# Kernel optimization log

Hardware: AMD Instinct MI355X
Metric: run time of the kernel (lower is better)

Reference implementation:

```python
import jax, jax.numpy as jnp
import numpy as np

V, B, P = 32, 128, 256   # views/directions, batch, max points per diagram
J = 75                   # n_elements (structure elements)
NF = 32                  # n_filters (= directions)
S2 = 25                  # stage_2_out
NU = 0.1
BN_EPS = 1e-5


def _transform(births, lifetimes):
    """UpperDiagonalThresholdedLogTransform(nu=0.1) on (birth, death) points."""
    deaths = births + lifetimes + 0.01
    inv = jnp.asarray(1.0 / np.sqrt(2.0), births.dtype)
    x = (births + deaths) * inv          # rotated 1st coord
    y = (deaths - births) * inv          # rotated 2nd coord (persistence), > 0
    y = jnp.where(y <= NU, jnp.log(y / NU) * NU + NU, y)
    return jnp.stack([x, y], axis=-1)    # [V,B,P,2]


def _batchnorm(x, gamma, beta, axis):
    mean = x.mean(axis=axis, keepdims=True)
    var = x.var(axis=axis, keepdims=True)  # biased, training-mode BN
    return (x - mean) / jnp.sqrt(var + BN_EPS) * gamma + beta


def setup_inputs() -> dict:
    key = jax.random.key(0)
    ks = jax.random.split(key, 20)
    inp = {
        "births": jax.random.uniform(ks[0], (V, B, P), jnp.float32),
        "lifetimes": jax.random.uniform(ks[1], (V, B, P), jnp.float32),
        "mask": jax.random.randint(ks[2], (V, B, P), 0, 2).astype(jnp.int32),
        # SLayerPHT params (one SLayer per view)
        "centers": jax.random.uniform(ks[3], (V, J, 2), jnp.float32),
        "sharpness": 4.0 + 0.1 * jax.random.normal(ks[4], (V, J, 2), jnp.float32),
        # stage_1: Conv1d(3->NF, k=1, no bias), Conv1d(NF->8, k=1, no bias)
        "w1": 0.1 * jax.random.normal(ks[5], (V, NF, 3), jnp.float32),
        "w2": 0.1 * jax.random.normal(ks[6], (V, 8, NF), jnp.float32),
        # stage_2: Linear(J->S2), BN(S2), Linear(S2->S2)
        "l1_w": 0.1 * jax.random.normal(ks[7], (V, S2, J), jnp.float32),
        "l1_b": 0.1 * jax.random.normal(ks[8], (V, S2), jnp.float32),
        "bn1_g": jnp.ones((V, S2), jnp.float32),
        "bn1_b": jnp.zeros((V, S2), jnp.float32),
        "l2_w": 0.1 * jax.random.normal(ks[9], (V, S2, S2), jnp.float32),
        "l2_b": 0.1 * jax.random.normal(ks[10], (V, S2), jnp.float32),
        # linear_1: Linear(V*S2 -> 500) + BN(500); linear_2: Linear(500 -> 200)
        "fc1_w": 0.05 * jax.random.normal(ks[11], (500, V * S2), jnp.float32),
        "fc1_b": 0.05 * jax.random.normal(ks[12], (500,), jnp.float32),
        "bn2_g": jnp.ones((500,), jnp.float32),
        "bn2_b": jnp.zeros((500,), jnp.float32),
        "fc2_w": 0.05 * jax.random.normal(ks[13], (200, 500), jnp.float32),
        "fc2_b": 0.05 * jax.random.normal(ks[14], (200,), jnp.float32),
    }
    return inp


def reference(births, lifetimes, mask, centers, sharpness, w1, w2,
              l1_w, l1_b, bn1_g, bn1_b, l2_w, l2_b,
              fc1_w, fc1_b, bn2_g, bn2_b, fc2_w, fc2_b):
    q = _transform(births, lifetimes)                 # [V,B,P,2]
    m = mask.astype(q.dtype)                          # [V,B,P]
    # SLayer: z[v,b,j] = sum_p m * exp(-sum_d s[v,j,d]^2 (q[v,b,p,d]-c[v,j,d])^2)
    s2 = sharpness * sharpness                        # [V,J,2]
    qa = jnp.concatenate([q * q, q, jnp.ones_like(q[..., :1])], axis=-1)  # [V,B,P,5]
    ca = jnp.concatenate([s2, -2.0 * s2 * centers,
                          (s2 * centers * centers).sum(-1, keepdims=True)], axis=-1)  # [V,J,5]
    d2 = jnp.einsum('vbpk,vjk->vbpj', qa, ca)         # squared weighted distance
    z = jnp.einsum('vbpj,vbp->vbj', jnp.exp(-d2), m)  # [V,B,J]
    # neighbor-direction stacking (n_neighbor_directions=1, cyclic): [i-1, i, i+1]
    zn = jnp.stack([jnp.roll(z, 1, axis=0), z, jnp.roll(z, -1, axis=0)], axis=2)  # [V,B,3,J]
    # stage_1: two 1x1 conv1d (no bias), then max over channels
    h = jnp.einsum('vbcj,vfc->vbfj', zn, w1)          # [V,B,NF,J]
    h = jnp.einsum('vbfj,vgf->vbgj', h, w2)           # [V,B,8,J]
    h = h.max(axis=2)                                 # [V,B,J]
    # stage_2: Linear -> BN(train) -> Linear -> ReLU (Dropout = eval identity)
    u = jnp.einsum('vbj,voj->vbo', h, l1_w) + l1_b[:, None, :]   # [V,B,S2]
    u = _batchnorm(u, bn1_g[:, None, :], bn1_b[:, None, :], axis=1)
    u = jnp.einsum('vbo,vpo->vbp', u, l2_w) + l2_b[:, None, :]
    u = jax.nn.relu(u)
    x = u.transpose(1, 0, 2).reshape(B, V * S2)       # torch.cat(x, 1)
    x = x @ fc1_w.T + fc1_b
    x = _batchnorm(x, bn2_g, bn2_b, axis=0)
    x = x @ fc2_w.T + fc2_b                           # [B,200]
    return x
```

## Files before the change

### kernel.cpp

```cpp
#include <hip/hip_runtime.h>

#define V 32
#define B 128
#define P 256
#define J 75
#define NF 32
#define S2 25
#define N1 500

__global__ __launch_bounds__(256) void slayer_kernel(
    const float* __restrict__ births,
    const float* __restrict__ lifetimes,
    const int* __restrict__ mask,
    const float* __restrict__ centers,
    const float* __restrict__ sharpness,
    float* __restrict__ z,
    float* __restrict__ acc_out)
{
    const int vb = blockIdx.x;
    const int v  = vb >> 7;
    const int tid = threadIdx.x;
    const int lane = tid & 63;

    {
        const int base = vb * 16;
        if (tid < 16 && base + tid < N1 * B) acc_out[base + tid] = 0.f;
    }

    __shared__ float4 pts[P];
    __shared__ int cnt;
    __shared__ float part[8 * J];

    if (tid == 0) cnt = 0;
    __syncthreads();

    const float inv = 0.70710678118654752f;
    {
        const int gi = vb * P + tid;
        float b0 = births[gi];
        float l0 = lifetimes[gi];
        int   m  = mask[gi];
        float d  = b0 + l0 + 0.01f;
        float x  = (b0 + d) * inv;
        float y  = (d - b0) * inv;
        if (y <= 0.1f) y = __logf(y * 10.0f) * 0.1f + 0.1f;

        bool keep = (m != 0);
        unsigned long long bal = __ballot(keep);
        unsigned long long lt  = (1ull << lane) - 1ull;
        int prefix = __popcll(bal & lt);
        int total  = __popcll(bal);
        int base = 0;
        if (lane == 0) base = atomicAdd(&cnt, total);
        base = __shfl(base, 0, 64);
        if (keep) pts[base + prefix] = make_float4(x, y, x * x, y * y);
    }
    __syncthreads();

    const int n = cnt;
    const int pid = tid >> 5;
    const int t32 = tid & 31;
    if (t32 < 25) {
        const int j0 = t32 * 3;
        float k0[3], k1[3], k2[3], k3[3], kc[3];
        #pragma unroll
        for (int c = 0; c < 3; ++c) {
            const int cj = (v * J + j0 + c) * 2;
            float cx = centers[cj + 0];
            float cy = centers[cj + 1];
            float sx = sharpness[cj + 0];
            float sy = sharpness[cj + 1];
            float s2x = sx * sx, s2y = sy * sy;
            k0[c] = -s2x;
            k1[c] = -s2y;
            k2[c] = 2.0f * s2x * cx;
            k3[c] = 2.0f * s2y * cy;
            kc[c] = -(s2x * cx * cx + s2y * cy * cy);
        }
        float a0 = 0.f, a1 = 0.f, a2 = 0.f;
        const int p0 = (n * pid) >> 3;
        const int p1 = (n * (pid + 1)) >> 3;
        #pragma unroll 2
        for (int p = p0; p < p1; ++p) {
            float4 a = pts[p];
            float d0 = fmaf(k0[0], a.z, kc[0]);
            d0 = fmaf(k1[0], a.w, d0); d0 = fmaf(k2[0], a.x, d0); d0 = fmaf(k3[0], a.y, d0);
            float d1 = fmaf(k0[1], a.z, kc[1]);
            d1 = fmaf(k1[1], a.w, d1); d1 = fmaf(k2[1], a.x, d1); d1 = fmaf(k3[1], a.y, d1);
            float d2 = fmaf(k0[2], a.z, kc[2]);
            d2 = fmaf(k1[2], a.w, d2); d2 = fmaf(k2[2], a.x, d2); d2 = fmaf(k3[2], a.y, d2);
            a0 += __expf(d0);
            a1 += __expf(d1);
            a2 += __expf(d2);
        }
        part[pid * J + j0 + 0] = a0;
        part[pid * J + j0 + 1] = a1;
        part[pid * J + j0 + 2] = a2;
    }
    __syncthreads();

    if (tid < J) {
        float s = 0.f;
        #pragma unroll
        for (int q = 0; q < 8; ++q) s += part[q * J + tid];
        z[vb * J + tid] = s;
    }
}

__global__ __launch_bounds__(1024) void stage2_kernel(
    const float* __restrict__ z,
    const float* __restrict__ w1,
    const float* __restrict__ w2,
    const float* __restrict__ l1_w,
    const float* __restrict__ l1_b,
    const float* __restrict__ bn1_g,
    const float* __restrict__ bn1_b,
    const float* __restrict__ l2_w,
    const float* __restrict__ l2_b,
    const float* __restrict__ fc1_w,
    float* __restrict__ acc_out)
{
    const int v   = blockIdx.x;
    const int tid = threadIdx.x;
    const int vm  = (v + V - 1) & (V - 1);
    const int vp  = (v + 1) & (V - 1);

    __shared__ float wcomb[8][3];
    __shared__ float l1ws[S2 * J];
    __shared__ float l1bs[S2];
    __shared__ float wl2[S2 * S2];
    __shared__ float l2bs[S2];
    __shared__ float hs[B * J];
    __shared__ float us[B * S2];
    __shared__ float xs[S2 * B];
    __shared__ float fw[N1 * S2];
    __shared__ float sred[32 * S2], ssred[32 * S2];
    __shared__ float sc[S2], sh[S2];

    if (tid < 24) {
        int g = tid / 3, c = tid - g * 3;
        const float* w2r = w2 + v * 8 * NF + g * NF;
        const float* w1c = w1 + v * NF * 3 + c;
        float s = 0.f;
        #pragma unroll
        for (int f = 0; f < NF; ++f) s += w2r[f] * w1c[f * 3];
        wcomb[g][c] = s;
    }
    for (int i = tid; i < S2 * J;  i += 1024) l1ws[i] = l1_w[v * S2 * J + i];
    for (int i = tid; i < S2 * S2; i += 1024) wl2[i]  = l2_w[v * S2 * S2 + i];
    for (int i = tid; i < N1 * S2; i += 1024) {
        int nn = i / S2, p = i - nn * S2;
        fw[i] = fc1_w[nn * (V * S2) + v * S2 + p];
    }
    if (tid < S2) { l1bs[tid] = l1_b[v * S2 + tid]; l2bs[tid] = l2_b[v * S2 + tid]; }
    __syncthreads();

    for (int t = tid; t < B * J; t += 1024) {
        float a0 = z[vm * (B * J) + t];
        float a1 = z[v  * (B * J) + t];
        float a2 = z[vp * (B * J) + t];
        float hm = -3.4e38f;
        #pragma unroll
        for (int g = 0; g < 8; ++g) {
            float s = wcomb[g][0] * a0 + wcomb[g][1] * a1 + wcomb[g][2] * a2;
            hm = fmaxf(hm, s);
        }
        hs[t] = hm;
    }
    __syncthreads();

    for (int t = tid; t < S2 * B; t += 1024) {
        int o = t >> 7;
        int b = t & 127;
        float acc = l1bs[o];
        const float* hrow = hs + b * J;
        const float* wrow = l1ws + o * J;
        #pragma unroll 5
        for (int j = 0; j < J; ++j) acc += hrow[j] * wrow[j];
        us[b * S2 + o] = acc;
    }
    __syncthreads();

    if (tid < 32 * S2) {
        int c = tid / S2;
        int o = tid - c * S2;
        float s = 0.f, ss = 0.f;
        #pragma unroll
        for (int b = c * 4; b < c * 4 + 4; ++b) {
            float x = us[b * S2 + o];
            s += x; ss += x * x;
        }
        sred[tid] = s; ssred[tid] = ss;
    }
    __syncthreads();

    if (tid < S2) {
        float s = 0.f, ss = 0.f;
        #pragma unroll
        for (int c = 0; c < 32; ++c) { s += sred[c * S2 + tid]; ss += ssred[c * S2 + tid]; }
        float mean = s * (1.f / B);
        float var  = ss * (1.f / B) - mean * mean;
        float istd = rsqrtf(var + 1e-5f);
        float g  = bn1_g[v * S2 + tid];
        float be = bn1_b[v * S2 + tid];
        sc[tid] = g * istd;
        sh[tid] = be - mean * g * istd;
    }
    __syncthreads();

    for (int i = tid; i < B * S2; i += 1024) {
        int o = i % S2;
        us[i] = us[i] * sc[o] + sh[o];
    }
    __syncthreads();

    for (int t = tid; t < S2 * B; t += 1024) {
        int p = t >> 7;
        int b = t & 127;
        float acc = l2bs[p];
        const float* urow = us + b * S2;
        const float* wrow = wl2 + p * S2;
        #pragma unroll
        for (int o = 0; o < S2; ++o) acc += urow[o] * wrow[o];
        xs[p * B + b] = fmaxf(acc, 0.f);
    }
    __syncthreads();

    for (int t = tid; t < N1 * B; t += 1024) {
        int nn = t >> 7;
        int b  = t & 127;
        const float* fr = fw + nn * S2;
        const float* xc = xs + b;
        float s = 0.f;
        #pragma unroll
        for (int p = 0; p < S2; ++p) s += fr[p] * xc[p * B];
        atomicAdd(&acc_out[nn * B + b], s);
    }
}

__global__ __launch_bounds__(256) void bn2_fc2_kernel(
    const float* __restrict__ acc_in,
    const float* __restrict__ fc1_b,
    const float* __restrict__ bn2_g,
    const float* __restrict__ bn2_b,
    const float* __restrict__ fc2_w,
    const float* __restrict__ fc2_b,
    float* __restrict__ out)
{
    const int k0  = blockIdx.x * 2;
    const int tid = threadIdx.x;

    __shared__ float w0s[N1], w1s[N1];
    __shared__ float fbs[N1];
    __shared__ float sred[2 * N1], ssred[2 * N1];
    __shared__ float scl[N1], shs[N1];
    __shared__ float pr0[B], pr1[B];

    for (int i = tid; i < N1; i += 256) {
        w0s[i] = fc2_w[k0 * N1 + i];
        w1s[i] = fc2_w[(k0 + 1) * N1 + i];
        fbs[i] = fc1_b[i];
    }
    __syncthreads();

    for (int idx = tid; idx < 2 * N1; idx += 256) {
        int nn = idx >> 1;
        int c  = idx & 1;
        const float* ap = acc_in + nn * B + c * 64;
        float fb = fbs[nn];
        float s = 0.f, ss = 0.f;
        #pragma unroll 8
        for (int j = 0; j < 64; ++j) {
            float x = ap[j] + fb;
            s += x; ss += x * x;
        }
        sred[idx] = s; ssred[idx] = ss;
    }
    __syncthreads();

    for (int nn = tid; nn < N1; nn += 256) {
        float s  = sred[2 * nn] + sred[2 * nn + 1];
        float ss = ssred[2 * nn] + ssred[2 * nn + 1];
        float mean = s * (1.f / B);
        float var  = ss * (1.f / B) - mean * mean;
        float istd = rsqrtf(var + 1e-5f);
        float g  = bn2_g[nn];
        float be = bn2_b[nn];
        scl[nn] = g * istd;
        shs[nn] = be - mean * g * istd;
    }
    __syncthreads();

    const int kk = tid >> 7;
    const int b  = tid & 127;
    float a0 = 0.f, a1 = 0.f;
    for (int nn = kk * 250; nn < kk * 250 + 250; ++nn) {
        float y = (acc_in[nn * B + b] + fbs[nn]) * scl[nn] + shs[nn];
        a0 += y * w0s[nn];
        a1 += y * w1s[nn];
    }
    if (kk == 1) { pr0[b] = a0; pr1[b] = a1; }
    __syncthreads();

    if (kk == 0) {
        out[b * 200 + k0]     = a0 + pr0[b] + fc2_b[k0];
        out[b * 200 + k0 + 1] = a1 + pr1[b] + fc2_b[k0 + 1];
    }
}

extern "C" void kernel_launch(void* const* d_in, const int* in_sizes, int n_in,
                              void* d_out, int out_size, void* d_ws, size_t ws_size,
                              hipStream_t stream) {
    const float* births    = (const float*)d_in[0];
    const float* lifetimes = (const float*)d_in[1];
    const int*   mask      = (const int*)d_in[2];
    const float* centers   = (const float*)d_in[3];
    const float* sharpness = (const float*)d_in[4];
    const float* w1        = (const float*)d_in[5];
    const float* w2        = (const float*)d_in[6];
    const float* l1_w      = (const float*)d_in[7];
    const float* l1_b      = (const float*)d_in[8];
    const float* bn1_g     = (const float*)d_in[9];
    const float* bn1_b     = (const float*)d_in[10];
    const float* l2_w      = (const float*)d_in[11];
    const float* l2_b      = (const float*)d_in[12];
    const float* fc1_w     = (const float*)d_in[13];
    const float* fc1_b     = (const float*)d_in[14];
    const float* bn2_g     = (const float*)d_in[15];
    const float* bn2_b     = (const float*)d_in[16];
    const float* fc2_w     = (const float*)d_in[17];
    const float* fc2_b     = (const float*)d_in[18];
    float* out = (float*)d_out;

    float* ws  = (float*)d_ws;
    float* z   = ws;
    float* acc = ws + 307200;

    slayer_kernel <<<V * B, 256, 0, stream>>>(births, lifetimes, mask, centers,
                                              sharpness, z, acc);
    stage2_kernel <<<V, 1024, 0, stream>>>(z, w1, w2, l1_w, l1_b, bn1_g, bn1_b,
                                           l2_w, l2_b, fc1_w, acc);
    bn2_fc2_kernel<<<100, 256, 0, stream>>>(acc, fc1_b, bn2_g, bn2_b,
                                            fc2_w, fc2_b, out);
}
```

Baseline: 173.0 us.

## Move fc1 out of per-view stage2 into separate fc1+BN and fc2 kernels

Stage2 now writes the per-view ReLU outputs to a transposed global buffer instead of doing its fc1 slice with 64K atomicAdds per block over 32 blocks. A new 250-block kernel computes fc1 for two output neurons each, including the full-batch BN via wave shuffles. A separate 200-block kernel does fc2. This removes atomics, the accumulator zeroing and the large per-view fc1 weight staging, and spreads the fc1 work over many more blocks, at the cost of an extra launch and an extra global round trip.

```diff
diff --git a/kernel.cpp b/kernel.cpp
--- a/kernel.cpp
+++ b/kernel.cpp
@@ -14,18 +14,12 @@
     const int* __restrict__ mask,
     const float* __restrict__ centers,
     const float* __restrict__ sharpness,
-    float* __restrict__ z,
-    float* __restrict__ acc_out)
+    float* __restrict__ z)
 {
     const int vb = blockIdx.x;
     const int v  = vb >> 7;
     const int tid = threadIdx.x;
     const int lane = tid & 63;
-
-    {
-        const int base = vb * 16;
-        if (tid < 16 && base + tid < N1 * B) acc_out[base + tid] = 0.f;
-    }
 
     __shared__ float4 pts[P];
     __shared__ int cnt;
@@ -117,8 +111,7 @@
     const float* __restrict__ bn1_b,
     const float* __restrict__ l2_w,
     const float* __restrict__ l2_b,
-    const float* __restrict__ fc1_w,
-    float* __restrict__ acc_out)
+    float* __restrict__ xT)
 {
     const int v   = blockIdx.x;
     const int tid = threadIdx.x;
@@ -132,8 +125,6 @@
     __shared__ float l2bs[S2];
     __shared__ float hs[B * J];
     __shared__ float us[B * S2];
-    __shared__ float xs[S2 * B];
-    __shared__ float fw[N1 * S2];
     __shared__ float sred[32 * S2], ssred[32 * S2];
     __shared__ float sc[S2], sh[S2];
 
@@ -148,10 +139,6 @@
     }
     for (int i = tid; i < S2 * J;  i += 1024) l1ws[i] = l1_w[v * S2 * J + i];
     for (int i = tid; i < S2 * S2; i += 1024) wl2[i]  = l2_w[v * S2 * S2 + i];
-    for (int i = tid; i < N1 * S2; i += 1024) {
-        int nn = i / S2, p = i - nn * S2;
-        fw[i] = fc1_w[nn * (V * S2) + v * S2 + p];
-    }
     if (tid < S2) { l1bs[tid] = l1_b[v * S2 + tid]; l2bs[tid] = l2_b[v * S2 + tid]; }
     __syncthreads();
 
@@ -222,90 +209,116 @@
         const float* wrow = wl2 + p * S2;
         #pragma unroll
         for (int o = 0; o < S2; ++o) acc += urow[o] * wrow[o];
-        xs[p * B + b] = fmaxf(acc, 0.f);
-    }
-    __syncthreads();
-
-    for (int t = tid; t < N1 * B; t += 1024) {
-        int nn = t >> 7;
-        int b  = t & 127;
-        const float* fr = fw + nn * S2;
-        const float* xc = xs + b;
-        float s = 0.f;
-        #pragma unroll
-        for (int p = 0; p < S2; ++p) s += fr[p] * xc[p * B];
-        atomicAdd(&acc_out[nn * B + b], s);
-    }
-}
-
-__global__ __launch_bounds__(256) void bn2_fc2_kernel(
-    const float* __restrict__ acc_in,
+        acc = fmaxf(acc, 0.f);
+        xT[(v * S2 + p) * B + b] = acc;
+    }
+}
+
+__global__ __launch_bounds__(256) void fc1_bn2_kernel(
+    const float* __restrict__ xT,
+    const float* __restrict__ fc1_w,
     const float* __restrict__ fc1_b,
     const float* __restrict__ bn2_g,
     const float* __restrict__ bn2_b,
+    float* __restrict__ y1n)
+{
+    const int n0  = blockIdx.x * 2;
+    const int tid = threadIdx.x;
+    const int kk  = tid >> 7;
+    const int b   = tid & 127;
+    const int K   = V * S2;
+
+    __shared__ float wsm[2][V * S2];
+    __shared__ float pr0[B], pr1[B];
+    __shared__ float red[2][2][2];
+
+    for (int i = tid; i < 2 * K; i += 256) {
+        int ni = i / K;
+        int k  = i - ni * K;
+        wsm[ni][k] = fc1_w[(n0 + ni) * K + k];
+    }
+    __syncthreads();
+
+    float a0 = 0.f, a1 = 0.f;
+    {
+        const float* xp = xT + kk * 400 * B + b;
+        const float* w0 = wsm[0] + kk * 400;
+        const float* w1p = wsm[1] + kk * 400;
+        for (int k = 0; k < 400; ++k) {
+            float xv = xp[k * B];
+            a0 += xv * w0[k];
+            a1 += xv * w1p[k];
+        }
+    }
+
+    if (kk == 1) { pr0[b] = a0; pr1[b] = a1; }
+    __syncthreads();
+
+    float t0 = 0.f, t1 = 0.f;
+    if (kk == 0) {
+        t0 = a0 + pr0[b] + fc1_b[n0];
+        t1 = a1 + pr1[b] + fc1_b[n0 + 1];
+        const int wave = tid >> 6;
+        const int lane = tid & 63;
+        float s0 = t0, q0 = t0 * t0;
+        float s1 = t1, q1 = t1 * t1;
+        #pragma unroll
+        for (int off = 32; off > 0; off >>= 1) {
+            s0 += __shfl_down(s0, off, 64);
+            q0 += __shfl_down(q0, off, 64);
+            s1 += __shfl_down(s1, off, 64);
+            q1 += __shfl_down(q1, off, 64);
+        }
+        if (lane == 0) {
+            red[wave][0][0] = s0; red[wave][1][0] = q0;
+            red[wave][0][1] = s1; red[wave][1][1] = q1;
+        }
+    }
+    __syncthreads();
+
+    if (kk == 0) {
+        #pragma unroll
+        for (int ni = 0; ni < 2; ++ni) {
+            float s  = red[0][0][ni] + red[1][0][ni];
+            float ss = red[0][1][ni] + red[1][1][ni];
+            float mean = s * (1.f / B);
+            float var  = ss * (1.f / B) - mean * mean;
+            float istd = rsqrtf(var + 1e-5f);
+            float g   = bn2_g[n0 + ni];
+            float be  = bn2_b[n0 + ni];
+            float scl = g * istd;
+            float t   = ni ? t1 : t0;
+            y1n[(n0 + ni) * B + b] = t * scl + (be - mean * scl);
+        }
+    }
+}
+
+__global__ __launch_bounds__(256) void fc2_kernel(
+    const float* __restrict__ y1n,
     const float* __restrict__ fc2_w,
     const float* __restrict__ fc2_b,
     float* __restrict__ out)
 {
-    const int k0  = blockIdx.x * 2;
+    const int n2 = blockIdx.x;
     const int tid = threadIdx.x;
-
-    __shared__ float w0s[N1], w1s[N1];
-    __shared__ float fbs[N1];
-    __shared__ float sred[2 * N1], ssred[2 * N1];
-    __shared__ float scl[N1], shs[N1];
-    __shared__ float pr0[B], pr1[B];
-
-    for (int i = tid; i < N1; i += 256) {
-        w0s[i] = fc2_w[k0 * N1 + i];
-        w1s[i] = fc2_w[(k0 + 1) * N1 + i];
-        fbs[i] = fc1_b[i];
-    }
-    __syncthreads();
-
-    for (int idx = tid; idx < 2 * N1; idx += 256) {
-        int nn = idx >> 1;
-        int c  = idx & 1;
-        const float* ap = acc_in + nn * B + c * 64;
-        float fb = fbs[nn];
-        float s = 0.f, ss = 0.f;
-        #pragma unroll 8
-        for (int j = 0; j < 64; ++j) {
-            float x = ap[j] + fb;
-            s += x; ss += x * x;
-        }
-        sred[idx] = s; ssred[idx] = ss;
-    }
-    __syncthreads();
-
-    for (int nn = tid; nn < N1; nn += 256) {
-        float s  = sred[2 * nn] + sred[2 * nn + 1];
-        float ss = ssred[2 * nn] + ssred[2 * nn + 1];
-        float mean = s * (1.f / B);
-        float var  = ss * (1.f / B) - mean * mean;
-        float istd = rsqrtf(var + 1e-5f);
-        float g  = bn2_g[nn];
-        float be = bn2_b[nn];
-        scl[nn] = g * istd;
-        shs[nn] = be - mean * g * istd;
-    }
-    __syncthreads();
-
     const int kk = tid >> 7;
     const int b  = tid & 127;
-    float a0 = 0.f, a1 = 0.f;
-    for (int nn = kk * 250; nn < kk * 250 + 250; ++nn) {
-        float y = (acc_in[nn * B + b] + fbs[nn]) * scl[nn] + shs[nn];
-        a0 += y * w0s[nn];
-        a1 += y * w1s[nn];
-    }
-    if (kk == 1) { pr0[b] = a0; pr1[b] = a1; }
-    __syncthreads();
-
-    if (kk == 0) {
-        out[b * 200 + k0]     = a0 + pr0[b] + fc2_b[k0];
-        out[b * 200 + k0 + 1] = a1 + pr1[b] + fc2_b[k0 + 1];
-    }
+
+    __shared__ float wsm[500];
+    __shared__ float pr[B];
+    for (int i = tid; i < 500; i += 256) wsm[i] = fc2_w[n2 * 500 + i];
+    __syncthreads();
+
+    float acc = 0.f;
+    const float* yp = y1n + kk * 250 * B + b;
+    const float* wp = wsm + kk * 250;
+    for (int k = 0; k < 250; ++k) acc += yp[k * B] * wp[k];
+
+    if (kk == 1) pr[b] = acc;
+    __syncthreads();
+
+    if (kk == 0)
+        out[b * 200 + n2] = acc + pr[b] + fc2_b[n2];
 }
 
 extern "C" void kernel_launch(void* const* d_in, const int* in_sizes, int n_in,
@@ -334,12 +347,13 @@
 
     float* ws  = (float*)d_ws;
     float* z   = ws;
-    float* acc = ws + 307200;
+    float* xT  = ws + 307200;
+    float* y1n = ws + 307200 + 102400;
 
     slayer_kernel <<<V * B, 256, 0, stream>>>(births, lifetimes, mask, centers,
-                                              sharpness, z, acc);
+                                              sharpness, z);
     stage2_kernel <<<V, 1024, 0, stream>>>(z, w1, w2, l1_w, l1_b, bn1_g, bn1_b,
-                                           l2_w, l2_b, fc1_w, acc);
-    bn2_fc2_kernel<<<100, 256, 0, stream>>>(acc, fc1_b, bn2_g, bn2_b,
-                                            fc2_w, fc2_b, out);
-}
+                                           l2_w, l2_b, xT);
+    fc1_bn2_kernel<<<250, 256, 0, stream>>>(xT, fc1_w, fc1_b, bn2_g, bn2_b, y1n);
+    fc2_kernel    <<<200, 256, 0, stream>>>(y1n, fc2_w, fc2_b, out);
+}
```

Measured after the change: 154.6 us. -10.6%, faster.
